# Kernel tuning notes

Hardware: AMD Instinct MI355X
Metric: run time of the kernel (lower is better)

Reference implementation:

```python
import jax, jax.numpy as jnp
import numpy as np

N = 8192      # nodes
IN_FEATS = 128
OUT_FEATS = 64
DEG = 16      # avg degree for random edges
NEG_SLOPE = 0.01  # nn.LeakyReLU default


def setup_inputs() -> dict:
    key = jax.random.key(0)
    k1, k2, k3, k4, k5, k6 = jax.random.split(key, 6)
    inputs = jax.random.normal(k1, (N, IN_FEATS), dtype=jnp.float32)
    # Random symmetric adjacency with self-loops (dense, as in the original module)
    us = jax.random.randint(k2, (N * DEG,), 0, N)
    vs = jax.random.randint(k3, (N * DEG,), 0, N)
    A = jnp.zeros((N, N), dtype=jnp.float32)
    A = A.at[us, vs].set(1.0)
    A = A.at[vs, us].set(1.0)
    idx = jnp.arange(N)
    A = A.at[idx, idx].set(1.0)
    # Linear layer params (torch nn.Linear: weight [out, in])
    W = jax.random.normal(k4, (OUT_FEATS, IN_FEATS), dtype=jnp.float32) * (1.0 / np.sqrt(IN_FEATS))
    b = jnp.zeros((OUT_FEATS,), dtype=jnp.float32)
    # attention params, torch.rand -> uniform [0,1)
    a1 = jax.random.uniform(k5, (1, OUT_FEATS), dtype=jnp.float32)
    a2 = jax.random.uniform(k6, (1, OUT_FEATS), dtype=jnp.float32)
    return {"inputs": inputs, "A": A, "W": W, "b": b, "a1": a1, "a2": a2}


def reference(inputs, A, W, b, a1, a2):
    z = inputs @ W.T + b                                  # [N, out]
    zi = jnp.sum(a1 * z, axis=1, keepdims=True)           # [N, 1]
    zj = jnp.sum(a2 * z, axis=1, keepdims=True)           # [N, 1]
    n = A.shape[0]
    idx = jnp.arange(n)
    diagA = jnp.diagonal(A)                               # A_ii
    # attention_A + attention_B = A*zi + diag(A_ii * zj)  (A*(eye*zj) only keeps diagonal)
    att = A * zi
    att = att.at[idx, idx].add(diagA * zj[:, 0])
    att = jax.nn.leaky_relu(att, NEG_SLOPE)
    att = jnp.exp(att) * A
    att = att / jnp.sum(att, axis=1, keepdims=True)       # row-normalize
    h = z - att @ z
    return jax.nn.relu(h)
```

## Files before the change

kernel.cpp:

```cpp
#include <hip/hip_runtime.h>
#include <math.h>

#define NN 8192
#define IN_F 128
#define OUT_F 64
#define NEG_SLOPE 0.01f
#define K1_ROWS 32

__global__ __launch_bounds__(256) void k1_linear(
    const float* __restrict__ X, const float* __restrict__ W,
    const float* __restrict__ b, const float* __restrict__ a1,
    const float* __restrict__ a2, float* __restrict__ z,
    float* __restrict__ ev, float* __restrict__ dv)
{
    __shared__ float Wl[OUT_F * 129];
    __shared__ float xs[K1_ROWS * IN_F];
    const int t = threadIdx.x;
    const int blk = blockIdx.x;

    for (int idx = t; idx < OUT_F * IN_F; idx += 256) {
        int f = idx >> 7, k = idx & 127;
        Wl[f * 129 + k] = W[idx];
    }
    {
        const float4* Xv = reinterpret_cast<const float4*>(X + (size_t)blk * (K1_ROWS * IN_F));
        float4* xsv = reinterpret_cast<float4*>(xs);
#pragma unroll
        for (int idx = t; idx < K1_ROWS * IN_F / 4; idx += 256)
            xsv[idx] = Xv[idx];
    }
    __syncthreads();

    const int wid = t >> 6;
    const int lane = t & 63;
    const float bias = b[lane];
    const float a1f = a1[lane], a2f = a2[lane];

#pragma unroll
    for (int r8 = 0; r8 < 8; ++r8) {
        const int row = wid * 8 + r8;
        float acc = 0.f;
#pragma unroll 8
        for (int k = 0; k < IN_F; ++k)
            acc = fmaf(xs[row * IN_F + k], Wl[lane * 129 + k], acc);
        const float zval = acc + bias;
        const int i = blk * K1_ROWS + row;
        z[i * OUT_F + lane] = zval;

        float p1 = a1f * zval;
        float p2 = a2f * zval;
#pragma unroll
        for (int off = 32; off > 0; off >>= 1) {
            p1 += __shfl_down(p1, off, 64);
            p2 += __shfl_down(p2, off, 64);
        }
        if (lane == 0) {
            const float s1 = p1;
            const float s2 = p1 + p2;
            const float l1 = s1 > 0.f ? s1 : NEG_SLOPE * s1;
            const float l2 = s2 > 0.f ? s2 : NEG_SLOPE * s2;
            ev[i] = expf(l1);
            dv[i] = expf(l2);
        }
    }
}

__global__ __launch_bounds__(256) void k2_row(
    const float* __restrict__ A, const float* __restrict__ z,
    const float* __restrict__ ev, const float* __restrict__ dv,
    float* __restrict__ out)
{
    __shared__ float accw[4][64];
    __shared__ float degw[4];

    const int i = blockIdx.x;
    const int t = threadIdx.x;
    const int wid = t >> 6, lane = t & 63;
    const float4* __restrict__ Arow =
        reinterpret_cast<const float4*>(A + (size_t)i * NN);

    float4 v[8];
#pragma unroll
    for (int c = 0; c < 8; ++c)
        v[c] = Arow[wid * 512 + c * 64 + lane];

    float acc = 0.f;
    float deg = 0.f;

#pragma unroll
    for (int c = 0; c < 8; ++c) {
        const float4 a4 = v[c];
        deg += a4.x + a4.y + a4.z + a4.w;
        const int jbase = wid * 2048 + c * 256;
        unsigned long long m;
        m = __ballot(a4.x != 0.f);
        while (m) { int l = __builtin_ctzll(m); m &= m - 1;
                    acc += z[(size_t)(jbase + l * 4 + 0) * OUT_F + lane]; }
        m = __ballot(a4.y != 0.f);
        while (m) { int l = __builtin_ctzll(m); m &= m - 1;
                    acc += z[(size_t)(jbase + l * 4 + 1) * OUT_F + lane]; }
        m = __ballot(a4.z != 0.f);
        while (m) { int l = __builtin_ctzll(m); m &= m - 1;
                    acc += z[(size_t)(jbase + l * 4 + 2) * OUT_F + lane]; }
        m = __ballot(a4.w != 0.f);
        while (m) { int l = __builtin_ctzll(m); m &= m - 1;
                    acc += z[(size_t)(jbase + l * 4 + 3) * OUT_F + lane]; }
    }

#pragma unroll
    for (int off = 32; off > 0; off >>= 1)
        deg += __shfl_down(deg, off, 64);
    if (lane == 0) degw[wid] = deg;
    accw[wid][lane] = acc;
    __syncthreads();

    if (t < 64) {
        const float degT = degw[0] + degw[1] + degw[2] + degw[3];
        const float sumNbr = accw[0][t] + accw[1][t] + accw[2][t] + accw[3][t];
        const float e = ev[i], d = dv[i];
        const float S = (degT - 1.f) * e + d;
        const float zif = z[(size_t)i * OUT_F + t];
        const float h = zif * (1.f + (e - d) / S) - (e / S) * sumNbr;
        out[(size_t)i * OUT_F + t] = h > 0.f ? h : 0.f;
    }
}

extern "C" void kernel_launch(void* const* d_in, const int* in_sizes, int n_in,
                              void* d_out, int out_size, void* d_ws, size_t ws_size,
                              hipStream_t stream) {
    const float* X  = (const float*)d_in[0];
    const float* A  = (const float*)d_in[1];
    const float* W  = (const float*)d_in[2];
    const float* b  = (const float*)d_in[3];
    const float* a1 = (const float*)d_in[4];
    const float* a2 = (const float*)d_in[5];
    float* out = (float*)d_out;

    float* ws = (float*)d_ws;
    float* z  = ws;
    float* ev = ws + NN * OUT_F;
    float* dv = ev + NN;

    k1_linear<<<NN / K1_ROWS, 256, 0, stream>>>(X, W, b, a1, a2, z, ev, dv);
    k2_row<<<NN, 256, 0, stream>>>(A, z, ev, dv, out);
}
```

Before: 72.12 us.

## Shrink k1 row tile, add occupancy hints, pack adjacency bits in k2

k1 now processes 8 rows per block instead of 32, giving four times as many blocks, and gains a min-blocks launch bound. k2 packs the nonzero flags of its 32 loaded A values into a bitmask and frees the float4 registers. Degree becomes a popcount, and neighbor z loads are issued two at a time for more memory-level parallelism. k2 also gets a min-blocks-per-CU hint of 6. The aim is higher occupancy and latency hiding, at the cost of reloading W for every smaller k1 block and possible register spills.

New measurement: 67.36 us. 1.07x faster.

```diff
diff --git a/kernel.cpp b/kernel.cpp
--- a/kernel.cpp
+++ b/kernel.cpp
@@ -5,9 +5,9 @@
 #define IN_F 128
 #define OUT_F 64
 #define NEG_SLOPE 0.01f
-#define K1_ROWS 32
+#define K1_ROWS 8
 
-__global__ __launch_bounds__(256) void k1_linear(
+__global__ __launch_bounds__(256, 4) void k1_linear(
     const float* __restrict__ X, const float* __restrict__ W,
     const float* __restrict__ b, const float* __restrict__ a1,
     const float* __restrict__ a2, float* __restrict__ z,
@@ -25,9 +25,7 @@
     {
         const float4* Xv = reinterpret_cast<const float4*>(X + (size_t)blk * (K1_ROWS * IN_F));
         float4* xsv = reinterpret_cast<float4*>(xs);
-#pragma unroll
-        for (int idx = t; idx < K1_ROWS * IN_F / 4; idx += 256)
-            xsv[idx] = Xv[idx];
+        if (t < K1_ROWS * IN_F / 4) xsv[t] = Xv[t];
     }
     __syncthreads();
 
@@ -37,8 +35,8 @@
     const float a1f = a1[lane], a2f = a2[lane];
 
 #pragma unroll
-    for (int r8 = 0; r8 < 8; ++r8) {
-        const int row = wid * 8 + r8;
+    for (int r2 = 0; r2 < 2; ++r2) {
+        const int row = wid * 2 + r2;
         float acc = 0.f;
 #pragma unroll 8
         for (int k = 0; k < IN_F; ++k)
@@ -65,13 +63,13 @@
     }
 }
 
-__global__ __launch_bounds__(256) void k2_row(
+__global__ __launch_bounds__(256, 6) void k2_row(
     const float* __restrict__ A, const float* __restrict__ z,
     const float* __restrict__ ev, const float* __restrict__ dv,
     float* __restrict__ out)
 {
     __shared__ float accw[4][64];
-    __shared__ float degw[4];
+    __shared__ int   degw[4];
 
     const int i = blockIdx.x;
     const int t = threadIdx.x;
@@ -84,27 +82,35 @@
     for (int c = 0; c < 8; ++c)
         v[c] = Arow[wid * 512 + c * 64 + lane];
 
-    float acc = 0.f;
-    float deg = 0.f;
-
+    unsigned int bits = 0;
 #pragma unroll
     for (int c = 0; c < 8; ++c) {
-        const float4 a4 = v[c];
-        deg += a4.x + a4.y + a4.z + a4.w;
-        const int jbase = wid * 2048 + c * 256;
-        unsigned long long m;
-        m = __ballot(a4.x != 0.f);
-        while (m) { int l = __builtin_ctzll(m); m &= m - 1;
-                    acc += z[(size_t)(jbase + l * 4 + 0) * OUT_F + lane]; }
-        m = __ballot(a4.y != 0.f);
-        while (m) { int l = __builtin_ctzll(m); m &= m - 1;
-                    acc += z[(size_t)(jbase + l * 4 + 1) * OUT_F + lane]; }
-        m = __ballot(a4.z != 0.f);
-        while (m) { int l = __builtin_ctzll(m); m &= m - 1;
-                    acc += z[(size_t)(jbase + l * 4 + 2) * OUT_F + lane]; }
-        m = __ballot(a4.w != 0.f);
-        while (m) { int l = __builtin_ctzll(m); m &= m - 1;
-                    acc += z[(size_t)(jbase + l * 4 + 3) * OUT_F + lane]; }
+        bits |= (v[c].x != 0.f ? 1u : 0u) << (c * 4 + 0);
+        bits |= (v[c].y != 0.f ? 1u : 0u) << (c * 4 + 1);
+        bits |= (v[c].z != 0.f ? 1u : 0u) << (c * 4 + 2);
+        bits |= (v[c].w != 0.f ? 1u : 0u) << (c * 4 + 3);
+    }
+    int deg = __popc(bits);
+
+    float acc = 0.f;
+#pragma unroll
+    for (int c = 0; c < 8; ++c) {
+#pragma unroll
+        for (int k = 0; k < 4; ++k) {
+            unsigned long long m = __ballot(((bits >> (c * 4 + k)) & 1u) != 0u);
+            const int jbase = wid * 2048 + c * 256 + k;
+            while (m) {
+                const int l0 = __builtin_ctzll(m); m &= m - 1;
+                if (m) {
+                    const int l1 = __builtin_ctzll(m); m &= m - 1;
+                    const float z0 = z[(size_t)(jbase + l0 * 4) * OUT_F + lane];
+                    const float z1 = z[(size_t)(jbase + l1 * 4) * OUT_F + lane];
+                    acc += z0 + z1;
+                } else {
+                    acc += z[(size_t)(jbase + l0 * 4) * OUT_F + lane];
+                }
+            }
+        }
     }
 
 #pragma unroll
@@ -115,7 +121,7 @@
     __syncthreads();
 
     if (t < 64) {
-        const float degT = degw[0] + degw[1] + degw[2] + degw[3];
+        const float degT = (float)(degw[0] + degw[1] + degw[2] + degw[3]);
         const float sumNbr = accw[0][t] + accw[1][t] + accw[2][t] + accw[3][t];
         const float e = ev[i], d = dv[i];
         const float S = (degT - 1.f) * e + d;
```
